# Optimization experiments

Hardware: AMD Instinct MI355X
Metric: run time of the kernel (lower is better)

Reference implementation:

```python
import jax, jax.numpy as jnp
import numpy as np

NEG_BIG = -9e15  # matches torch's -9000000000000000.0 mask value


def setup_inputs() -> dict:
    key = jax.random.key(0)
    k0, k1, k2, k3 = jax.random.split(key, 4)
    B, N, F_IN, F_OUT = 8, 2048, 128, 128
    h = jax.random.normal(k0, (B, N, F_IN), dtype=jnp.float32)
    adj = jax.random.randint(k1, (B, N, N), 0, 2, dtype=jnp.int32)
    W = jax.random.normal(k2, (F_IN, F_OUT), dtype=jnp.float32) * 0.05
    a = jax.random.normal(k3, (2 * F_OUT,), dtype=jnp.float32) * 0.05
    return {"h": h, "adj": adj, "W": W, "a": a}


def reference(h, adj, W, a):
    # Wh: [B, N, F_out]
    Wh = jnp.einsum("bnf,fo->bno", h, W)
    f_out = Wh.shape[-1]
    # a @ [Wh_i || Wh_j] == (a1 @ Wh_i) + (a2 @ Wh_j): avoids O(N^2 * 2F) concat
    a1, a2 = a[:f_out], a[f_out:]
    src = jnp.einsum("bno,o->bn", Wh, a1)  # row (i) contribution
    dst = jnp.einsum("bno,o->bn", Wh, a2)  # col (j) contribution
    e = jax.nn.leaky_relu(src[:, :, None] + dst[:, None, :], negative_slope=0.2)
    e = jnp.where(adj > 0, e, NEG_BIG)
    attention = jax.nn.softmax(e, axis=-1)  # dropout is identity at eval time
    h_prime = jnp.einsum("bij,bjo->bio", attention, Wh)
    return h_prime
```

## Files before the change

### kernel.cpp

```cpp
#include <hip/hip_runtime.h>
#include <hip/hip_bf16.h>

#define BB 8
#define NN 2048
#define FF 128

typedef __bf16 bf16x8 __attribute__((ext_vector_type(8)));
typedef float f32x4 __attribute__((ext_vector_type(4)));
typedef float f32x16 __attribute__((ext_vector_type(16)));

__device__ __forceinline__ void gload_lds16(const void* g, void* l) {
    __builtin_amdgcn_global_load_lds(
        (const __attribute__((address_space(1))) unsigned int*)g,
        (__attribute__((address_space(3))) unsigned int*)l, 16, 0, 0);
}

__global__ __launch_bounds__(256) void wh_kernel(
    const float* __restrict__ h, const float* __restrict__ W,
    const float* __restrict__ a, __bf16* __restrict__ fragB,
    float* __restrict__ srcg, float* __restrict__ dstg)
{
    __shared__ float  s_h[32][132];
    __shared__ __bf16 s_wh[32][132];
    __shared__ float  s_s[2][32];
    __shared__ float  s_d[2][32];

    const int bid = blockIdx.x;
    const int b   = bid >> 6;
    const int J   = bid & 63;
    const int r0  = J * 32;
    const int t   = threadIdx.x;
    const int w   = t >> 6;
    const int l   = t & 63;
    const int itile = w & 1;
    const int fh    = w >> 1;
    const int g     = l >> 4;
    const int c16   = l & 15;

#pragma unroll
    for (int i = 0; i < 4; ++i) {
        const int idx = t + i * 256;
        const int r   = idx >> 5;
        const int c4  = idx & 31;
        *(f32x4*)&s_h[r][c4 * 4] =
            *(const f32x4*)(h + (size_t)(b * NN + r0 + r) * FF + c4 * 4);
    }
    __syncthreads();

    const float* hrow = &s_h[itile * 16 + c16][0];
    f32x4 acc[4] = {};

#pragma unroll
    for (int kt = 0; kt < 4; ++kt) {
        const int k0 = kt * 32 + g * 8;
        f32x4 h0 = *(const f32x4*)(hrow + k0);
        f32x4 h1 = *(const f32x4*)(hrow + k0 + 4);
        bf16x8 af;
        af[0]=(__bf16)h0[0]; af[1]=(__bf16)h0[1]; af[2]=(__bf16)h0[2]; af[3]=(__bf16)h0[3];
        af[4]=(__bf16)h1[0]; af[5]=(__bf16)h1[1]; af[6]=(__bf16)h1[2]; af[7]=(__bf16)h1[3];
#pragma unroll
        for (int ft = 0; ft < 4; ++ft) {
            const int c = (fh * 4 + ft) * 16 + c16;
            bf16x8 bf;
#pragma unroll
            for (int e = 0; e < 8; ++e) bf[e] = (__bf16)W[(k0 + e) * FF + c];
            acc[ft] = __builtin_amdgcn_mfma_f32_16x16x32_bf16(af, bf, acc[ft], 0, 0, 0);
        }
    }

    float a1v[4], a2v[4];
#pragma unroll
    for (int ft = 0; ft < 4; ++ft) {
        const int c = (fh * 4 + ft) * 16 + c16;
        a1v[ft] = a[c];
        a2v[ft] = a[FF + c];
    }
#pragma unroll
    for (int r = 0; r < 4; ++r) {
        float s = 0.f, d2 = 0.f;
#pragma unroll
        for (int ft = 0; ft < 4; ++ft) {
            s  += acc[ft][r] * a1v[ft];
            d2 += acc[ft][r] * a2v[ft];
        }
#pragma unroll
        for (int m = 1; m <= 8; m <<= 1) {
            s  += __shfl_xor(s,  m);
            d2 += __shfl_xor(d2, m);
        }
        if (c16 == 0) {
            s_s[fh][itile * 16 + g * 4 + r] = s;
            s_d[fh][itile * 16 + g * 4 + r] = d2;
        }
    }

#pragma unroll
    for (int ft = 0; ft < 4; ++ft)
#pragma unroll
        for (int r = 0; r < 4; ++r)
            s_wh[itile * 16 + g * 4 + r][(fh * 4 + ft) * 16 + c16] = (__bf16)acc[ft][r];

    __syncthreads();

#pragma unroll
    for (int e2 = 0; e2 < 2; ++e2) {
        const int ent  = t + e2 * 256;
        const int tile = ent >> 6;
        const int jl   = tile >> 2;
        const int ft   = tile & 3;
        const int lE   = ent & 63;
        const int rowE = jl * 16 + (lE >> 5) * 8;
        const int colE = ft * 32 + (lE & 31);
        bf16x8 v;
#pragma unroll
        for (int ee = 0; ee < 8; ++ee) v[ee] = s_wh[rowE + ee][colE];
        *(bf16x8*)(fragB + (((size_t)(b * 128 + J * 2 + jl) * 4 + ft) * 64 + lE) * 8) = v;
    }

    if (t < 32) {
        srcg[b * NN + r0 + t] = s_s[0][t] + s_s[1][t];
        dstg[b * NN + r0 + t] = s_d[0][t] + s_d[1][t];
    }
}

__global__ __launch_bounds__(256, 2) void attn_kernel(
    const int* __restrict__ adj, const __bf16* __restrict__ fragB,
    const float* __restrict__ srcg, const float* __restrict__ dstg,
    float* __restrict__ out)
{
    __shared__ char s_all[74240];

    const int bid0 = blockIdx.x;
    const int bid  = (bid0 & 7) * 64 + (bid0 >> 3);
    const int b    = bid >> 6;
    const int I0   = (bid & 63) * 32;
    const int t    = threadIdx.x;
    const int q    = t >> 6;
    const int l    = t & 63;
    const int r31  = l & 31;
    const int hi   = l >> 5;

    char* awave = s_all + q * 16384;
    char* dstw  = s_all + 65536 + q * 2048;
    float* s_ps = (float*)(s_all + 73728);

    const float sv = srcg[b * NN + I0 + r31];
    asm volatile("s_waitcnt vmcnt(0) lgkmcnt(0)" ::: "memory");

    const char* aSrc = (const char*)adj
        + ((size_t)(b * NN + I0 + r31) * NN + q * 512) * 4 + hi * 16;
    const char* fBase = (const char*)fragB
        + (size_t)(b * 128 + q * 32) * 4096 + (size_t)l * 16;
    const char* dSrc = (const char*)(dstg + (size_t)b * NN + q * 512) + l * 16;

#define ISSUE_A(ki_) {                                                        \
        const char* pa_ = aSrc + (size_t)(ki_) * 128;                         \
        char* ad_ = awave + ((ki_) & 3) * 4096 + l * 16;                      \
        gload_lds16(pa_,      ad_);                                           \
        gload_lds16(pa_ + 32, ad_ + 1024);                                    \
        gload_lds16(pa_ + 64, ad_ + 2048);                                    \
        gload_lds16(pa_ + 96, ad_ + 3072); }

#define ISSUE_F(ki_, B0_, B1_, B2_, B3_, B4_, B5_, B6_, B7_) {                \
        const char* p0_ = fBase + (size_t)(ki_) * 8192;                       \
        const char* p1_ = p0_ + 4096;                                         \
        asm volatile("global_load_dwordx4 %0, %1, off"                        \
                     : "=&v"(B0_) : "v"(p0_));                                \
        asm volatile("global_load_dwordx4 %0, %1, off offset:1024"            \
                     : "=&v"(B1_) : "v"(p0_));                                \
        asm volatile("global_load_dwordx4 %0, %1, off offset:2048"            \
                     : "=&v"(B2_) : "v"(p0_));                                \
        asm volatile("global_load_dwordx4 %0, %1, off offset:3072"            \
                     : "=&v"(B3_) : "v"(p0_));                                \
        asm volatile("global_load_dwordx4 %0, %1, off"                        \
                     : "=&v"(B4_) : "v"(p1_));                                \
        asm volatile("global_load_dwordx4 %0, %1, off offset:1024"            \
                     : "=&v"(B5_) : "v"(p1_));                                \
        asm volatile("global_load_dwordx4 %0, %1, off offset:2048"            \
                     : "=&v"(B6_) : "v"(p1_));                                \
        asm volatile("global_load_dwordx4 %0, %1, off offset:3072"            \
                     : "=&v"(B7_) : "v"(p1_)); }

    bf16x8 Fa0, Fa1, Fa2, Fa3, Fa4, Fa5, Fa6, Fa7;
    bf16x8 Fb0, Fb1, Fb2, Fb3, Fb4, Fb5, Fb6, Fb7;
    f32x16 acc0 = {}, acc1 = {}, acc2 = {}, acc3 = {};
    float psum = 0.f;

    gload_lds16(dSrc,        dstw + l * 16);
    gload_lds16(dSrc + 1024, dstw + 1024 + l * 16);
    ISSUE_A(0);
    ISSUE_F(0, Fa0, Fa1, Fa2, Fa3, Fa4, Fa5, Fa6, Fa7);
    ISSUE_A(1);

#define STEP(kt_, C0_,C1_,C2_,C3_,C4_,C5_,C6_,C7_, N0_,N1_,N2_,N3_,N4_,N5_,N6_,N7_) { \
        const int kF_ = ((kt_) + 1 < 16) ? (kt_) + 1 : 15;                    \
        const int kA_ = ((kt_) + 2 < 16) ? (kt_) + 2 : 15;                    \
        ISSUE_F(kF_, N0_, N1_, N2_, N3_, N4_, N5_, N6_, N7_);                 \
        ISSUE_A(kA_);                                                         \
        asm volatile("s_waitcnt vmcnt(16)" ::: "memory");                     \
              \
        const char* ab_ = awave + ((kt_) & 3) * 4096 + hi * 1024 + r31 * 16;  \
        const int4 A00_ = *(const int4*)(ab_);                                \
        const int4 A01_ = *(const int4*)(ab_ + 512);                          \
        const int4 A10_ = *(const int4*)(ab_ + 2048);                         \
        const int4 A11_ = *(const int4*)(ab_ + 2048 + 512);                   \
        const f32x4 d00_ = *(const f32x4*)(dstw + (kt_) * 128 + hi * 32);     \
        const f32x4 d01_ = *(const f32x4*)(dstw + (kt_) * 128 + hi * 32 + 16);\
        const f32x4 d10_ = *(const f32x4*)(dstw + (kt_) * 128 + 64 + hi * 32);\
        const f32x4 d11_ = *(const f32x4*)(dstw + (kt_) * 128 + 64 + hi * 32 + 16);\
        const int   am0_[8] = {A00_.x, A00_.y, A00_.z, A00_.w,                \
                               A01_.x, A01_.y, A01_.z, A01_.w};               \
        const int   am1_[8] = {A10_.x, A10_.y, A10_.z, A10_.w,                \
                               A11_.x, A11_.y, A11_.z, A11_.w};               \
        const float dv0_[8] = {d00_[0], d00_[1], d00_[2], d00_[3],            \
                               d01_[0], d01_[1], d01_[2], d01_[3]};           \
        const float dv1_[8] = {d10_[0], d10_[1], d10_[2], d10_[3],            \
                               d11_[0], d11_[1], d11_[2], d11_[3]};           \
        bf16x8 af0_, af1_;                                                    \
        _Pragma("unroll")                                                     \
        for (int e = 0; e < 8; ++e) {                                         \
            float x0 = sv + dv0_[e];                                          \
            x0 = fmaxf(x0, 0.2f * x0);                                        \
            float p0 = __expf(x0);                                            \
            p0 = (am0_[e] > 0) ? p0 : 0.f;                                    \
            psum += p0;                                                       \
            af0_[e] = (__bf16)p0;                                             \
            float x1 = sv + dv1_[e];                                          \
            x1 = fmaxf(x1, 0.2f * x1);                                        \
            float p1 = __expf(x1);                                            \
            p1 = (am1_[e] > 0) ? p1 : 0.f;                                    \
            psum += p1;                                                       \
            af1_[e] = (__bf16)p1;                                             \
        }                                                                     \
        acc0 = __builtin_amdgcn_mfma_f32_32x32x16_bf16(af0_, C0_, acc0, 0, 0, 0); \
        acc1 = __builtin_amdgcn_mfma_f32_32x32x16_bf16(af0_, C1_, acc1, 0, 0, 0); \
        acc2 = __builtin_amdgcn_mfma_f32_32x32x16_bf16(af0_, C2_, acc2, 0, 0, 0); \
        acc3 = __builtin_amdgcn_mfma_f32_32x32x16_bf16(af0_, C3_, acc3, 0, 0, 0); \
        acc0 = __builtin_amdgcn_mfma_f32_32x32x16_bf16(af1_, C4_, acc0, 0, 0, 0); \
        acc1 = __builtin_amdgcn_mfma_f32_32x32x16_bf16(af1_, C5_, acc1, 0, 0, 0); \
        acc2 = __builtin_amdgcn_mfma_f32_32x32x16_bf16(af1_, C6_, acc2, 0, 0, 0); \
        acc3 = __builtin_amdgcn_mfma_f32_32x32x16_bf16(af1_, C7_, acc3, 0, 0, 0); }

    for (int kt2 = 0; kt2 < 16; kt2 += 2) {
        STEP(kt2 + 0, Fa0,Fa1,Fa2,Fa3,Fa4,Fa5,Fa6,Fa7, Fb0,Fb1,Fb2,Fb3,Fb4,Fb5,Fb6,Fb7);
        STEP(kt2 + 1, Fb0,Fb1,Fb2,Fb3,Fb4,Fb5,Fb6,Fb7, Fa0,Fa1,Fa2,Fa3,Fa4,Fa5,Fa6,Fa7);
    }
#undef STEP
#undef ISSUE_A
#undef ISSUE_F

    asm volatile("s_waitcnt vmcnt(0) lgkmcnt(0)" ::: "memory");

    psum += __shfl_xor(psum, 32);
    if (l < 32) s_ps[q * 32 + l] = psum;

    __syncthreads();
    float* comb = (float*)s_all;
    {
        float* cb = comb + ((q * 4 + 0) * 64 + l) * 17;
#pragma unroll
        for (int r = 0; r < 16; ++r) cb[r] = acc0[r];
        cb = comb + ((q * 4 + 1) * 64 + l) * 17;
#pragma unroll
        for (int r = 0; r < 16; ++r) cb[r] = acc1[r];
        cb = comb + ((q * 4 + 2) * 64 + l) * 17;
#pragma unroll
        for (int r = 0; r < 16; ++r) cb[r] = acc2[r];
        cb = comb + ((q * 4 + 3) * 64 + l) * 17;
#pragma unroll
        for (int r = 0; r < 16; ++r) cb[r] = acc3[r];
    }
    __syncthreads();

    f32x16 tot;
#pragma unroll
    for (int r = 0; r < 16; ++r)
        tot[r] = comb[((0 * 4 + q) * 64 + l) * 17 + r]
               + comb[((1 * 4 + q) * 64 + l) * 17 + r]
               + comb[((2 * 4 + q) * 64 + l) * 17 + r]
               + comb[((3 * 4 + q) * 64 + l) * 17 + r];

    const float dtot = s_ps[0 * 32 + r31] + s_ps[1 * 32 + r31]
                     + s_ps[2 * 32 + r31] + s_ps[3 * 32 + r31];
    const float rin  = 1.f / dtot;

#pragma unroll
    for (int r = 0; r < 16; ++r) {
        const int row  = (r & 3) + 8 * (r >> 2) + 4 * hi;
        const float dv2 = __shfl(rin, row);
        out[(size_t)(b * NN + I0 + row) * FF + q * 32 + r31] = tot[r] * dv2;
    }
}

extern "C" void kernel_launch(void* const* d_in, const int* in_sizes, int n_in,
                              void* d_out, int out_size, void* d_ws, size_t ws_size,
                              hipStream_t stream)
{
    const float* h   = (const float*)d_in[0];
    const int*   adj = (const int*)d_in[1];
    const float* W   = (const float*)d_in[2];
    const float* a   = (const float*)d_in[3];
    float* out = (float*)d_out;

    char* ws = (char*)d_ws;
    __bf16* fragB = (__bf16*)ws;
    float*  srcg  = (float*)(ws + (4 << 20));
    float*  dstg  = (float*)(ws + (4 << 20) + (64 << 10));

    wh_kernel<<<512, 256, 0, stream>>>(h, W, a, fragB, srcg, dstg);
    attn_kernel<<<512, 256, 0, stream>>>(adj, fragB, srcg, dstg, out);
}
```

Measured before the change: 43.84 us.

## Restructure adj tile loading with swizzled shared LDS and stage W transposed

```diff
diff --git a/kernel.cpp b/kernel.cpp
--- a/kernel.cpp
+++ b/kernel.cpp
@@ -22,6 +22,7 @@
 {
     __shared__ float  s_h[32][132];
     __shared__ __bf16 s_wh[32][132];
+    __shared__ __bf16 s_Wt[128][136];
     __shared__ float  s_s[2][32];
     __shared__ float  s_d[2][32];
 
@@ -45,6 +46,19 @@
         *(f32x4*)&s_h[r][c4 * 4] =
             *(const f32x4*)(h + (size_t)(b * NN + r0 + r) * FF + c4 * 4);
     }
+    {
+        const int wk  = t >> 1;
+        const int wc0 = (t & 1) * 64;
+        const float* wrow = W + wk * FF + wc0;
+#pragma unroll
+        for (int i = 0; i < 16; ++i) {
+            const f32x4 v = *(const f32x4*)(wrow + i * 4);
+            s_Wt[wc0 + i * 4 + 0][wk] = (__bf16)v[0];
+            s_Wt[wc0 + i * 4 + 1][wk] = (__bf16)v[1];
+            s_Wt[wc0 + i * 4 + 2][wk] = (__bf16)v[2];
+            s_Wt[wc0 + i * 4 + 3][wk] = (__bf16)v[3];
+        }
+    }
     __syncthreads();
 
     const float* hrow = &s_h[itile * 16 + c16][0];
@@ -61,9 +75,7 @@
 #pragma unroll
         for (int ft = 0; ft < 4; ++ft) {
             const int c = (fh * 4 + ft) * 16 + c16;
-            bf16x8 bf;
-#pragma unroll
-            for (int e = 0; e < 8; ++e) bf[e] = (__bf16)W[(k0 + e) * FF + c];
+            const bf16x8 bf = *(const bf16x8*)&s_Wt[c][k0];
             acc[ft] = __builtin_amdgcn_mfma_f32_16x16x32_bf16(af, bf, acc[ft], 0, 0, 0);
         }
     }
@@ -139,30 +151,37 @@
     const int l    = t & 63;
     const int r31  = l & 31;
     const int hi   = l >> 5;
-
-    char* awave = s_all + q * 16384;
-    char* dstw  = s_all + 65536 + q * 2048;
+    const int xr   = l & 7;
+
+    float* dstf = (float*)(s_all + 65536);
     float* s_ps = (float*)(s_all + 73728);
 
     const float sv = srcg[b * NN + I0 + r31];
     asm volatile("s_waitcnt vmcnt(0) lgkmcnt(0)" ::: "memory");
 
-    const char* aSrc = (const char*)adj
-        + ((size_t)(b * NN + I0 + r31) * NN + q * 512) * 4 + hi * 16;
-    const char* fBase = (const char*)fragB
-        + (size_t)(b * 128 + q * 32) * 4096 + (size_t)l * 16;
-    const char* dSrc = (const char*)(dstg + (size_t)b * NN + q * 512) + l * 16;
-
-#define ISSUE_A(ki_) {                                                        \
-        const char* pa_ = aSrc + (size_t)(ki_) * 128;                         \
-        char* ad_ = awave + ((ki_) & 3) * 4096 + l * 16;                      \
-        gload_lds16(pa_,      ad_);                                           \
-        gload_lds16(pa_ + 32, ad_ + 1024);                                    \
-        gload_lds16(pa_ + 64, ad_ + 2048);                                    \
-        gload_lds16(pa_ + 96, ad_ + 3072); }
-
-#define ISSUE_F(ki_, B0_, B1_, B2_, B3_, B4_, B5_, B6_, B7_) {                \
-        const char* p0_ = fBase + (size_t)(ki_) * 8192;                       \
+    const char* adjBB = (const char*)adj + (size_t)b * NN * (NN * 4);
+    const int ro0 = 2 * (q * 4 + 0) + hi;
+    const int ro1 = 2 * (q * 4 + 1) + hi;
+    const int ro2 = 2 * (q * 4 + 2) + hi;
+    const int ro3 = 2 * (q * 4 + 3) + hi;
+    const char* aB0 = adjBB + (size_t)(I0 + ro0) * (NN * 4) + ((r31 ^ (ro0 & 7)) * 16);
+    const char* aB1 = adjBB + (size_t)(I0 + ro1) * (NN * 4) + ((r31 ^ (ro1 & 7)) * 16);
+    const char* aB2 = adjBB + (size_t)(I0 + ro2) * (NN * 4) + ((r31 ^ (ro2 & 7)) * 16);
+    const char* aB3 = adjBB + (size_t)(I0 + ro3) * (NN * 4) + ((r31 ^ (ro3 & 7)) * 16);
+    const char* fB = (const char*)fragB + ((size_t)(b * 128 + q * 2) * 4096)
+                     + (size_t)l * 16;
+    const char* dS = (const char*)(dstg + (size_t)b * NN) + q * 2048 + l * 16;
+
+#define ISSUE_A(w_, sl_) {                                                    \
+        const size_t wo_ = (size_t)(w_) * 512;                                \
+        char* ds_ = s_all + (sl_) * 16384 + q * 4096 + l * 16;                \
+        gload_lds16(aB0 + wo_, ds_);                                          \
+        gload_lds16(aB1 + wo_, ds_ + 1024);                                   \
+        gload_lds16(aB2 + wo_, ds_ + 2048);                                   \
+        gload_lds16(aB3 + wo_, ds_ + 3072); }
+
+#define ISSUE_F(w_, B0_,B1_,B2_,B3_,B4_,B5_,B6_,B7_) {                        \
+        const char* p0_ = fB + (size_t)(w_) * 32768;                          \
         const char* p1_ = p0_ + 4096;                                         \
         asm volatile("global_load_dwordx4 %0, %1, off"                        \
                      : "=&v"(B0_) : "v"(p0_));                                \
@@ -186,28 +205,30 @@
     f32x16 acc0 = {}, acc1 = {}, acc2 = {}, acc3 = {};
     float psum = 0.f;
 
-    gload_lds16(dSrc,        dstw + l * 16);
-    gload_lds16(dSrc + 1024, dstw + 1024 + l * 16);
-    ISSUE_A(0);
+    gload_lds16(dS,        (char*)dstf + q * 2048 + l * 16);
+    gload_lds16(dS + 1024, (char*)dstf + q * 2048 + 1024 + l * 16);
+    ISSUE_A(0, 0);
     ISSUE_F(0, Fa0, Fa1, Fa2, Fa3, Fa4, Fa5, Fa6, Fa7);
-    ISSUE_A(1);
-
-#define STEP(kt_, C0_,C1_,C2_,C3_,C4_,C5_,C6_,C7_, N0_,N1_,N2_,N3_,N4_,N5_,N6_,N7_) { \
-        const int kF_ = ((kt_) + 1 < 16) ? (kt_) + 1 : 15;                    \
-        const int kA_ = ((kt_) + 2 < 16) ? (kt_) + 2 : 15;                    \
-        ISSUE_F(kF_, N0_, N1_, N2_, N3_, N4_, N5_, N6_, N7_);                 \
-        ISSUE_A(kA_);                                                         \
-        asm volatile("s_waitcnt vmcnt(16)" ::: "memory");                     \
-              \
-        const char* ab_ = awave + ((kt_) & 3) * 4096 + hi * 1024 + r31 * 16;  \
-        const int4 A00_ = *(const int4*)(ab_);                                \
-        const int4 A01_ = *(const int4*)(ab_ + 512);                          \
-        const int4 A10_ = *(const int4*)(ab_ + 2048);                         \
-        const int4 A11_ = *(const int4*)(ab_ + 2048 + 512);                   \
-        const f32x4 d00_ = *(const f32x4*)(dstw + (kt_) * 128 + hi * 32);     \
-        const f32x4 d01_ = *(const f32x4*)(dstw + (kt_) * 128 + hi * 32 + 16);\
-        const f32x4 d10_ = *(const f32x4*)(dstw + (kt_) * 128 + 64 + hi * 32);\
-        const f32x4 d11_ = *(const f32x4*)(dstw + (kt_) * 128 + 64 + hi * 32 + 16);\
+
+#define STEP(w_, C0_,C1_,C2_,C3_,C4_,C5_,C6_,C7_, N0_,N1_,N2_,N3_,N4_,N5_,N6_,N7_) { \
+        const int wn_ = ((w_) + 1 < 16) ? (w_) + 1 : 15;                      \
+        ISSUE_F(wn_, N0_, N1_, N2_, N3_, N4_, N5_, N6_, N7_);                 \
+        ISSUE_A(wn_, wn_ & 3);                                                \
+        asm volatile("s_waitcnt vmcnt(12)" ::: "memory");                     \
+        __builtin_amdgcn_sched_barrier(0);                                    \
+        __builtin_amdgcn_s_barrier();                                         \
+        const char* as_ = s_all + ((w_) & 3) * 16384 + r31 * 512;             \
+        const int cqa_ = q * 8 + hi * 2;                                      \
+        const int cqb_ = cqa_ + 4;                                            \
+        const int4 A00_ = *(const int4*)(as_ + ((cqa_ ^ xr) * 16));           \
+        const int4 A01_ = *(const int4*)(as_ + (((cqa_ + 1) ^ xr) * 16));     \
+        const int4 A10_ = *(const int4*)(as_ + ((cqb_ ^ xr) * 16));           \
+        const int4 A11_ = *(const int4*)(as_ + (((cqb_ + 1) ^ xr) * 16));     \
+        const float* dw_ = dstf + (w_) * 128 + q * 32 + hi * 8;               \
+        const f32x4 d00_ = *(const f32x4*)(dw_);                              \
+        const f32x4 d01_ = *(const f32x4*)(dw_ + 4);                          \
+        const f32x4 d10_ = *(const f32x4*)(dw_ + 16);                         \
+        const f32x4 d11_ = *(const f32x4*)(dw_ + 20);                         \
         const int   am0_[8] = {A00_.x, A00_.y, A00_.z, A00_.w,                \
                                A01_.x, A01_.y, A01_.z, A01_.w};               \
         const int   am1_[8] = {A10_.x, A10_.y, A10_.z, A10_.w,                \
@@ -241,9 +262,11 @@
         acc2 = __builtin_amdgcn_mfma_f32_32x32x16_bf16(af1_, C6_, acc2, 0, 0, 0); \
         acc3 = __builtin_amdgcn_mfma_f32_32x32x16_bf16(af1_, C7_, acc3, 0, 0, 0); }
 
-    for (int kt2 = 0; kt2 < 16; kt2 += 2) {
-        STEP(kt2 + 0, Fa0,Fa1,Fa2,Fa3,Fa4,Fa5,Fa6,Fa7, Fb0,Fb1,Fb2,Fb3,Fb4,Fb5,Fb6,Fb7);
-        STEP(kt2 + 1, Fb0,Fb1,Fb2,Fb3,Fb4,Fb5,Fb6,Fb7, Fa0,Fa1,Fa2,Fa3,Fa4,Fa5,Fa6,Fa7);
+    for (int w2 = 0; w2 < 16; w2 += 2) {
+        STEP(w2 + 0, Fa0,Fa1,Fa2,Fa3,Fa4,Fa5,Fa6,Fa7,
+                     Fb0,Fb1,Fb2,Fb3,Fb4,Fb5,Fb6,Fb7);
+        STEP(w2 + 1, Fb0,Fb1,Fb2,Fb3,Fb4,Fb5,Fb6,Fb7,
+                     Fa0,Fa1,Fa2,Fa3,Fa4,Fa5,Fa6,Fa7);
     }
 #undef STEP
 #undef ISSUE_A
@@ -254,31 +277,42 @@
     psum += __shfl_xor(psum, 32);
     if (l < 32) s_ps[q * 32 + l] = psum;
 
-    __syncthreads();
     float* comb = (float*)s_all;
+    f32x16 tot;
+
+    __syncthreads();
     {
-        float* cb = comb + ((q * 4 + 0) * 64 + l) * 17;
-#pragma unroll
-        for (int r = 0; r < 16; ++r) cb[r] = acc0[r];
-        cb = comb + ((q * 4 + 1) * 64 + l) * 17;
-#pragma unroll
-        for (int r = 0; r < 16; ++r) cb[r] = acc1[r];
-        cb = comb + ((q * 4 + 2) * 64 + l) * 17;
-#pragma unroll
-        for (int r = 0; r < 16; ++r) cb[r] = acc2[r];
-        cb = comb + ((q * 4 + 3) * 64 + l) * 17;
-#pragma unroll
-        for (int r = 0; r < 16; ++r) cb[r] = acc3[r];
-    }
-    __syncthreads();
-
-    f32x16 tot;
-#pragma unroll
-    for (int r = 0; r < 16; ++r)
-        tot[r] = comb[((0 * 4 + q) * 64 + l) * 17 + r]
-               + comb[((1 * 4 + q) * 64 + l) * 17 + r]
-               + comb[((2 * 4 + q) * 64 + l) * 17 + r]
-               + comb[((3 * 4 + q) * 64 + l) * 17 + r];
+        float* c0 = comb + ((q * 2 + 0) * 64 + l) * 17;
+        float* c1 = comb + ((q * 2 + 1) * 64 + l) * 17;
+#pragma unroll
+        for (int r = 0; r < 16; ++r) { c0[r] = acc0[r]; c1[r] = acc1[r]; }
+    }
+    __syncthreads();
+    if (q < 2) {
+#pragma unroll
+        for (int r = 0; r < 16; ++r)
+            tot[r] = comb[((0 * 2 + q) * 64 + l) * 17 + r]
+                   + comb[((1 * 2 + q) * 64 + l) * 17 + r]
+                   + comb[((2 * 2 + q) * 64 + l) * 17 + r]
+                   + comb[((3 * 2 + q) * 64 + l) * 17 + r];
+    }
+    __syncthreads();
+    {
+        float* c0 = comb + ((q * 2 + 0) * 64 + l) * 17;
+        float* c1 = comb + ((q * 2 + 1) * 64 + l) * 17;
+#pragma unroll
+        for (int r = 0; r < 16; ++r) { c0[r] = acc2[r]; c1[r] = acc3[r]; }
+    }
+    __syncthreads();
+    if (q >= 2) {
+        const int f2 = q - 2;
+#pragma unroll
+        for (int r = 0; r < 16; ++r)
+            tot[r] = comb[((0 * 2 + f2) * 64 + l) * 17 + r]
+                   + comb[((1 * 2 + f2) * 64 + l) * 17 + r]
+                   + comb[((2 * 2 + f2) * 64 + l) * 17 + r]
+                   + comb[((3 * 2 + f2) * 64 + l) * 17 + r];
+    }
 
     const float dtot = s_ps[0 * 32 + r31] + s_ps[1 * 32 + r31]
                      + s_ps[2 * 32 + r31] + s_ps[3 * 32 + r31];
```

Result: faster. 39.83 us (-9.1%).
